# Kernel optimization log

Measured on AMD Instinct MI355X. Metric: run time of the kernel, lower is better.

## Reference

```python
import jax, jax.numpy as jnp
import numpy as np

N_NODES = 100000
N_EDGES = 3200000
IN_CH = 512
HIDDEN = 64
LOC_OUT = 16
OUT_CH = 40


def setup_inputs() -> dict:
    key = jax.random.key(0)
    ks = jax.random.split(key, 10)
    return {
        "batch_x": jax.random.normal(ks[0], (N_NODES, IN_CH), dtype=jnp.float32),
        "edge_index": jax.random.randint(ks[1], (2, N_EDGES), 0, N_NODES, dtype=jnp.int64),
        "glob_emb": jax.random.normal(ks[2], (N_NODES, LOC_OUT), dtype=jnp.float32),
        "W1": jax.random.normal(ks[3], (IN_CH, HIDDEN), dtype=jnp.float32) * (1.0 / np.sqrt(IN_CH)),
        "b1": jnp.zeros((HIDDEN,), dtype=jnp.float32),
        "W2": jax.random.normal(ks[4], (HIDDEN, LOC_OUT), dtype=jnp.float32) * (1.0 / np.sqrt(HIDDEN)),
        "b2": jnp.zeros((LOC_OUT,), dtype=jnp.float32),
        "att_w1": jax.random.normal(ks[5], (LOC_OUT, 16), dtype=jnp.float32) * 0.25,
        "att_b1": jnp.zeros((16,), dtype=jnp.float32),
        "att_w2": jax.random.normal(ks[6], (16, 1), dtype=jnp.float32) * 0.25,
        "lin1_w": jax.random.normal(ks[7], (LOC_OUT, OUT_CH), dtype=jnp.float32) * 0.25,
        "lin1_b": jnp.zeros((OUT_CH,), dtype=jnp.float32),
    }


def _gcn_conv(x, W, b, row, col, n):
    # GCNConv: out = D^-1/2 (A + I) D^-1/2 (X W) + b   (PyG default: self-loops, sym norm)
    h = x @ W
    loops = jnp.arange(n, dtype=row.dtype)
    row2 = jnp.concatenate([row, loops])  # sources (x_j)
    col2 = jnp.concatenate([col, loops])  # targets (aggregation index)
    deg = jax.ops.segment_sum(jnp.ones_like(col2, dtype=h.dtype), col2, num_segments=n)
    dinv = jax.lax.rsqrt(jnp.maximum(deg, 1.0))  # deg >= 1 thanks to self-loops
    norm = dinv[row2] * dinv[col2]               # [E+N]
    agg = jax.ops.segment_sum(h[row2] * norm[:, None], col2, num_segments=n)
    return agg + b


def reference(batch_x, edge_index, glob_emb, W1, b1, W2, b2, att_w1, att_b1, att_w2, lin1_w, lin1_b):
    n = batch_x.shape[0]
    row, col = edge_index[0], edge_index[1]
    x = _gcn_conv(batch_x, W1, b1, row, col, n)
    x = jax.nn.relu(x)  # dropout p=0.0 -> identity
    x = _gcn_conv(x, W2, b2, row, col, n)  # last layer: no relu/dropout
    z = jnp.stack([x, glob_emb], axis=1)  # [N, 2, 16]
    w = jnp.tanh(z @ att_w1 + att_b1) @ att_w2  # [N, 2, 1]
    beta = jax.nn.softmax(w, axis=1)
    emb = jnp.sum(beta * z, axis=1)  # [N, 16]
    return emb @ lin1_w + lin1_b  # [N, 40]
```

## Files before the change

### kernel.cpp

```cpp
#include <hip/hip_runtime.h>

#define N_IN 512
#define HID 64
#define NBLK 256

typedef __attribute__((ext_vector_type(4))) float f32x4;
typedef __attribute__((ext_vector_type(8))) short bf16x8;

__device__ inline float bf2f(unsigned short s) {
    union { unsigned int u; float f; } v; v.u = ((unsigned int)s) << 16; return v.f;
}
__device__ inline unsigned short f2bf(float f) {
    union { float f; unsigned int u; } v; v.f = f;
    unsigned int u = v.u;
    return (unsigned short)((u + 0x7FFFu + ((u >> 16) & 1u)) >> 16);
}

__global__ void k_detect(const int* __restrict__ EI, int* __restrict__ flag) {
    if (threadIdx.x == 0 && blockIdx.x == 0)
        *flag = (EI[1] == 0 && EI[3] == 0 && EI[5] == 0 && EI[7] == 0) ? 1 : 0;
}

__global__ __launch_bounds__(256) void k_histA(const int* __restrict__ EI, const int* __restrict__ flag,
                                               int* __restrict__ hist, int E, int N, int K) {
    extern __shared__ int hs[];
    for (int k = threadIdx.x; k < K; k += 256) hs[k] = 0;
    __syncthreads();
    int chunk = (E + NBLK - 1) / NBLK;
    int s = blockIdx.x * chunk, e = min(E, s + chunk);
    bool f = (*flag) != 0;
    for (int i = s + threadIdx.x; i < e; i += 256) {
        int c = f ? ((const int2*)EI)[E + i].x : EI[E + i];
        if ((unsigned)c < (unsigned)N) atomicAdd(&hs[c >> 8], 1);
    }
    __syncthreads();
    for (int k = threadIdx.x; k < K; k += 256) hist[k * NBLK + blockIdx.x] = hs[k];
}

__global__ __launch_bounds__(256) void k_scan_a2(const int* __restrict__ in, int* __restrict__ out,
                                                 int* __restrict__ bsum, int n) {
    __shared__ int sd[256];
    int i = blockIdx.x * 256 + threadIdx.x;
    int v = (i < n) ? in[i] : 0;
    sd[threadIdx.x] = v;
    __syncthreads();
    for (int off = 1; off < 256; off <<= 1) {
        int t = 0;
        if (threadIdx.x >= (unsigned)off) t = sd[threadIdx.x - off];
        __syncthreads();
        sd[threadIdx.x] += t;
        __syncthreads();
    }
    if (i < n) out[i] = sd[threadIdx.x] - v;
    if (threadIdx.x == 255) bsum[blockIdx.x] = sd[255];
}

__global__ __launch_bounds__(512) void k_scan_b(const int* __restrict__ bsum, int* __restrict__ bexc, int nb) {
    __shared__ int sd[512];
    int t = threadIdx.x;
    int v = (t < nb) ? bsum[t] : 0;
    sd[t] = v;
    __syncthreads();
    for (int off = 1; off < 512; off <<= 1) {
        int u = 0;
        if (t >= off) u = sd[t - off];
        __syncthreads();
        sd[t] += u;
        __syncthreads();
    }
    if (t < nb) bexc[t] = sd[t] - v;
    if (t == 511) bexc[nb] = sd[511];
}

__global__ __launch_bounds__(256) void k_scan_c2(const int* __restrict__ bexc, int* __restrict__ out,
                                                 int n, int nb) {
    int i = blockIdx.x * 256 + threadIdx.x;
    if (i < n) out[i] += bexc[blockIdx.x];
    if (i == 0) out[n] = bexc[nb];
}

__global__ __launch_bounds__(256) void k_partB(const int* __restrict__ EI, const int* __restrict__ flag,
                                               const int* __restrict__ histS, int* __restrict__ edges2,
                                               int E, int N, int K) {
    extern __shared__ int cur[];
    for (int k = threadIdx.x; k < K; k += 256) cur[k] = histS[k * NBLK + blockIdx.x];
    __syncthreads();
    int chunk = (E + NBLK - 1) / NBLK;
    int s = blockIdx.x * chunk, e = min(E, s + chunk);
    bool f = (*flag) != 0;
    for (int i = s + threadIdx.x; i < e; i += 256) {
        int r, c;
        if (f) { const int2* E2 = (const int2*)EI; r = E2[i].x; c = E2[E + i].x; }
        else   { r = EI[i]; c = EI[E + i]; }
        if ((unsigned)r >= (unsigned)N || (unsigned)c >= (unsigned)N) continue;
        int pos = atomicAdd(&cur[c >> 8], 1);
        edges2[pos] = r | ((c & 255) << 20);
    }
}

__global__ __launch_bounds__(256) void k_bucket(const int* __restrict__ histS, const int* __restrict__ edges2,
                                                int* __restrict__ edges, int* __restrict__ start,
                                                float* __restrict__ dinv, int N, int NBtot) {
    __shared__ int hist[256], sd[256], cur[256];
    int b = blockIdx.x, tid = threadIdx.x;
    int base = histS[b * NBLK];
    int end  = histS[(b + 1) * NBLK];
    hist[tid] = 0;
    __syncthreads();
    for (int i = base + tid; i < end; i += 256)
        atomicAdd(&hist[(edges2[i] >> 20) & 255], 1);
    __syncthreads();
    int v = hist[tid];
    sd[tid] = v;
    __syncthreads();
    for (int off = 1; off < 256; off <<= 1) {
        int t = 0;
        if (tid >= off) t = sd[tid - off];
        __syncthreads();
        sd[tid] += t;
        __syncthreads();
    }
    int excl = sd[tid] - v;
    cur[tid] = excl;
    int node = b * 256 + tid;
    if (node < N) {
        start[node] = base + excl;
        dinv[node] = rsqrtf((float)(v + 1));
    }
    if (b == 0 && tid == 0) start[N] = histS[NBtot];
    __syncthreads();
    for (int i = base + tid; i < end; i += 256) {
        int pv = edges2[i];
        int pos = atomicAdd(&cur[(pv >> 20) & 255], 1);
        edges[base + pos] = pv & 0xFFFFF;
    }
}

__global__ __launch_bounds__(256) void k_wt(const float* __restrict__ W, unsigned short* __restrict__ Wt) {
    int i = blockIdx.x * 256 + threadIdx.x;
    int k = i >> 6, n = i & 63;
    Wt[n * 512 + k] = f2bf(W[i]);
}

__global__ __launch_bounds__(256) void k_gemm1(const float* __restrict__ X, const unsigned short* __restrict__ Wt,
                                               const float* __restrict__ dinv, unsigned short* __restrict__ H, int N) {
    int tid = threadIdx.x;
    int w = tid >> 6, lane = tid & 63;
    int m_l = lane & 15, q = lane >> 4;
    int m0 = blockIdx.x * 128 + w * 32;
    int rA0 = m0 + m_l, rA1 = m0 + 16 + m_l;
    int rc0 = rA0 < N ? rA0 : N - 1;
    int rc1 = rA1 < N ? rA1 : N - 1;
    const float* baseA0 = X + (size_t)rc0 * 512 + q * 8;
    const float* baseA1 = X + (size_t)rc1 * 512 + q * 8;
    const unsigned short* baseB = Wt + (size_t)m_l * 512 + q * 8;

    f32x4 acc[2][4] = {};
#pragma unroll 4
    for (int c = 0; c < 16; ++c) {
        int ko = c * 32;
        float4 x0a = *(const float4*)(baseA0 + ko);
        float4 x0b = *(const float4*)(baseA0 + ko + 4);
        float4 x1a = *(const float4*)(baseA1 + ko);
        float4 x1b = *(const float4*)(baseA1 + ko + 4);
        bf16x8 a0, a1;
        a0[0] = (short)f2bf(x0a.x); a0[1] = (short)f2bf(x0a.y); a0[2] = (short)f2bf(x0a.z); a0[3] = (short)f2bf(x0a.w);
        a0[4] = (short)f2bf(x0b.x); a0[5] = (short)f2bf(x0b.y); a0[6] = (short)f2bf(x0b.z); a0[7] = (short)f2bf(x0b.w);
        a1[0] = (short)f2bf(x1a.x); a1[1] = (short)f2bf(x1a.y); a1[2] = (short)f2bf(x1a.z); a1[3] = (short)f2bf(x1a.w);
        a1[4] = (short)f2bf(x1b.x); a1[5] = (short)f2bf(x1b.y); a1[6] = (short)f2bf(x1b.z); a1[7] = (short)f2bf(x1b.w);
#pragma unroll
        for (int t = 0; t < 4; ++t) {
            bf16x8 b = *(const bf16x8*)(baseB + (size_t)t * 16 * 512 + ko);
            acc[0][t] = __builtin_amdgcn_mfma_f32_16x16x32_bf16(a0, b, acc[0][t], 0, 0, 0);
            acc[1][t] = __builtin_amdgcn_mfma_f32_16x16x32_bf16(a1, b, acc[1][t], 0, 0, 0);
        }
    }
#pragma unroll
    for (int h = 0; h < 2; ++h) {
#pragma unroll
        for (int rg = 0; rg < 4; ++rg) {
            int row = m0 + h * 16 + q * 4 + rg;
            if (row < N) {
                float dv = dinv[row];
#pragma unroll
                for (int t = 0; t < 4; ++t)
                    H[(size_t)row * 64 + t * 16 + m_l] = f2bf(acc[h][t][rg] * dv);
            }
        }
    }
}

__global__ __launch_bounds__(256) void k_agg1(const unsigned short* __restrict__ H, const int* __restrict__ edges,
                                              const int* __restrict__ start, const float* __restrict__ dinv,
                                              const float* __restrict__ b1, unsigned short* __restrict__ X1, int N) {
    int wid = blockIdx.x * 4 + (threadIdx.x >> 6);
    int lane = threadIdx.x & 63;
    if (wid >= N) return;
    int g = lane >> 4;
    int c4 = lane & 15;
    const size_t coff = (size_t)c4 * 4;
    float a0 = 0.f, a1 = 0.f, a2 = 0.f, a3 = 0.f;
    int s = start[wid], e = start[wid + 1];
    int i = s;
    if ((i & 3) && i < e) {
        int lim = min(e, (i + 3) & ~3);
        int j = i + g;
        if (j < lim) {
            uint2 v = *(const uint2*)(H + (size_t)edges[j] * 64 + coff);
            a0 += __uint_as_float(v.x << 16);
            a1 += __uint_as_float(v.x & 0xffff0000u);
            a2 += __uint_as_float(v.y << 16);
            a3 += __uint_as_float(v.y & 0xffff0000u);
        }
        i = lim;
    }
    for (; i + 16 <= e; i += 16) {
        int4 sv = *(const int4*)(edges + i + g * 4);
        uint2 v0 = *(const uint2*)(H + (size_t)sv.x * 64 + coff);
        uint2 v1 = *(const uint2*)(H + (size_t)sv.y * 64 + coff);
        uint2 v2 = *(const uint2*)(H + (size_t)sv.z * 64 + coff);
        uint2 v3 = *(const uint2*)(H + (size_t)sv.w * 64 + coff);
        a0 += __uint_as_float(v0.x << 16) + __uint_as_float(v1.x << 16)
            + __uint_as_float(v2.x << 16) + __uint_as_float(v3.x << 16);
        a1 += __uint_as_float(v0.x & 0xffff0000u) + __uint_as_float(v1.x & 0xffff0000u)
            + __uint_as_float(v2.x & 0xffff0000u) + __uint_as_float(v3.x & 0xffff0000u);
        a2 += __uint_as_float(v0.y << 16) + __uint_as_float(v1.y << 16)
            + __uint_as_float(v2.y << 16) + __uint_as_float(v3.y << 16);
        a3 += __uint_as_float(v0.y & 0xffff0000u) + __uint_as_float(v1.y & 0xffff0000u)
            + __uint_as_float(v2.y & 0xffff0000u) + __uint_as_float(v3.y & 0xffff0000u);
    }
    for (; i < e; i += 4) {
        int j = i + g;
        if (j < e) {
            uint2 v = *(const uint2*)(H + (size_t)edges[j] * 64 + coff);
            a0 += __uint_as_float(v.x << 16);
            a1 += __uint_as_float(v.x & 0xffff0000u);
            a2 += __uint_as_float(v.y << 16);
            a3 += __uint_as_float(v.y & 0xffff0000u);
        }
    }
    a0 += __shfl_xor(a0, 16, 64); a0 += __shfl_xor(a0, 32, 64);
    a1 += __shfl_xor(a1, 16, 64); a1 += __shfl_xor(a1, 32, 64);
    a2 += __shfl_xor(a2, 16, 64); a2 += __shfl_xor(a2, 32, 64);
    a3 += __shfl_xor(a3, 16, 64); a3 += __shfl_xor(a3, 32, 64);
    if (g == 0) {
        float dv = dinv[wid];
        uint2 sv = *(const uint2*)(H + (size_t)wid * 64 + coff);
        a0 += __uint_as_float(sv.x << 16);
        a1 += __uint_as_float(sv.x & 0xffff0000u);
        a2 += __uint_as_float(sv.y << 16);
        a3 += __uint_as_float(sv.y & 0xffff0000u);
        float4 bv = *(const float4*)(b1 + c4 * 4);
        ushort4 o;
        o.x = f2bf(fmaxf(a0 * dv + bv.x, 0.f));
        o.y = f2bf(fmaxf(a1 * dv + bv.y, 0.f));
        o.z = f2bf(fmaxf(a2 * dv + bv.z, 0.f));
        o.w = f2bf(fmaxf(a3 * dv + bv.w, 0.f));
        *(ushort4*)(X1 + (size_t)wid * 64 + coff) = o;
    }
}

__global__ __launch_bounds__(256) void k_gemm2(const unsigned short* __restrict__ X1, const float* __restrict__ W2,
                                               const float* __restrict__ dinv, unsigned short* __restrict__ H2, int N) {
    __shared__ float Ws[1024];
    __shared__ float Xs[64][68];
    int tid = threadIdx.x;
    for (int i = tid; i < 1024; i += 256) Ws[i] = W2[i];
    int m0 = blockIdx.x * 64;
#pragma unroll
    for (int j = 0; j < 4; ++j) {
        int f = (j * 256 + tid) * 4;
        int r = f >> 6, k = f & 63;
        uint2 v = make_uint2(0u, 0u);
        if (m0 + r < N) v = *(const uint2*)(X1 + (size_t)(m0 + r) * 64 + k);
        Xs[r][k + 0] = bf2f((unsigned short)(v.x & 0xffffu));
        Xs[r][k + 1] = bf2f((unsigned short)(v.x >> 16));
        Xs[r][k + 2] = bf2f((unsigned short)(v.y & 0xffffu));
        Xs[r][k + 3] = bf2f((unsigned short)(v.y >> 16));
    }
    __syncthreads();
    int r = tid >> 2, cq = tid & 3;
    float acc0 = 0.f, acc1 = 0.f, acc2 = 0.f, acc3 = 0.f;
#pragma unroll 8
    for (int k = 0; k < 64; ++k) {
        float xv = Xs[r][k];
        const float* wp = &Ws[k * 16 + cq * 4];
        acc0 += xv * wp[0]; acc1 += xv * wp[1]; acc2 += xv * wp[2]; acc3 += xv * wp[3];
    }
    int m = m0 + r;
    if (m < N) {
        float dv = dinv[m];
        ushort4 o; o.x = f2bf(acc0 * dv); o.y = f2bf(acc1 * dv); o.z = f2bf(acc2 * dv); o.w = f2bf(acc3 * dv);
        *(ushort4*)(H2 + (size_t)m * 16 + cq * 4) = o;
    }
}

__global__ __launch_bounds__(256) void k_agg2(const unsigned short* __restrict__ H2, const int* __restrict__ edges,
                                              const int* __restrict__ start, const float* __restrict__ dinv,
                                              const float* __restrict__ b2, float* __restrict__ X2, int N) {
    int wid = blockIdx.x * 4 + (threadIdx.x >> 6);
    int lane = threadIdx.x & 63;
    if (wid >= N) return;
    int g = lane >> 3;
    int c2 = lane & 7;
    const size_t coff = (size_t)c2 * 2;
    float a0 = 0.f, a1 = 0.f;
    int s = start[wid], e = start[wid + 1];
    int i = s;
    if ((i & 3) && i < e) {
        int lim = min(e, (i + 3) & ~3);
        int j = i + g;
        if (j < lim) {
            unsigned int v = *(const unsigned int*)(H2 + (size_t)edges[j] * 16 + coff);
            a0 += __uint_as_float(v << 16);
            a1 += __uint_as_float(v & 0xffff0000u);
        }
        i = lim;
    }
    for (; i + 32 <= e; i += 32) {
        int4 sv = *(const int4*)(edges + i + g * 4);
        unsigned int v0 = *(const unsigned int*)(H2 + (size_t)sv.x * 16 + coff);
        unsigned int v1 = *(const unsigned int*)(H2 + (size_t)sv.y * 16 + coff);
        unsigned int v2 = *(const unsigned int*)(H2 + (size_t)sv.z * 16 + coff);
        unsigned int v3 = *(const unsigned int*)(H2 + (size_t)sv.w * 16 + coff);
        a0 += __uint_as_float(v0 << 16) + __uint_as_float(v1 << 16)
            + __uint_as_float(v2 << 16) + __uint_as_float(v3 << 16);
        a1 += __uint_as_float(v0 & 0xffff0000u) + __uint_as_float(v1 & 0xffff0000u)
            + __uint_as_float(v2 & 0xffff0000u) + __uint_as_float(v3 & 0xffff0000u);
    }
    for (; i < e; i += 8) {
        int j = i + g;
        if (j < e) {
            unsigned int v = *(const unsigned int*)(H2 + (size_t)edges[j] * 16 + coff);
            a0 += __uint_as_float(v << 16);
            a1 += __uint_as_float(v & 0xffff0000u);
        }
    }
    a0 += __shfl_xor(a0, 8, 64); a0 += __shfl_xor(a0, 16, 64); a0 += __shfl_xor(a0, 32, 64);
    a1 += __shfl_xor(a1, 8, 64); a1 += __shfl_xor(a1, 16, 64); a1 += __shfl_xor(a1, 32, 64);
    if (g == 0) {
        float dv = dinv[wid];
        unsigned int sv = *(const unsigned int*)(H2 + (size_t)wid * 16 + coff);
        a0 += __uint_as_float(sv << 16);
        a1 += __uint_as_float(sv & 0xffff0000u);
        float2 bv = *(const float2*)(b2 + c2 * 2);
        float2 o; o.x = a0 * dv + bv.x; o.y = a1 * dv + bv.y;
        *(float2*)(X2 + (size_t)wid * 16 + coff) = o;
    }
}

__global__ __launch_bounds__(256) void k_head(const float* __restrict__ X2, const float* __restrict__ G,
                                              const float* __restrict__ AW1, const float* __restrict__ AB1,
                                              const float* __restrict__ AW2, const float* __restrict__ LW,
                                              const float* __restrict__ LB, float* __restrict__ OUT, int N) {
    __shared__ float s_aw1[256], s_ab1[16], s_aw2[16], s_lw[640], s_lb[40];
    int tid = threadIdx.x;
    s_aw1[tid] = AW1[tid];
    if (tid < 16) { s_ab1[tid] = AB1[tid]; s_aw2[tid] = AW2[tid]; }
    for (int i = tid; i < 640; i += 256) s_lw[i] = LW[i];
    if (tid < 40) s_lb[tid] = LB[tid];
    __syncthreads();
    int node = blockIdx.x * 256 + tid;
    if (node >= N) return;
    float x[16], g[16];
    const float4* xp = (const float4*)(X2 + (size_t)node * 16);
    const float4* gp = (const float4*)(G + (size_t)node * 16);
#pragma unroll
    for (int q = 0; q < 4; ++q) {
        float4 v = xp[q]; x[q*4] = v.x; x[q*4+1] = v.y; x[q*4+2] = v.z; x[q*4+3] = v.w;
        float4 u = gp[q]; g[q*4] = u.x; g[q*4+1] = u.y; g[q*4+2] = u.z; g[q*4+3] = u.w;
    }
    float wx = 0.f, wg = 0.f;
#pragma unroll
    for (int j = 0; j < 16; ++j) {
        float tx = s_ab1[j], tg = s_ab1[j];
#pragma unroll
        for (int c = 0; c < 16; ++c) { tx += x[c] * s_aw1[c*16 + j]; tg += g[c] * s_aw1[c*16 + j]; }
        wx += tanhf(tx) * s_aw2[j];
        wg += tanhf(tg) * s_aw2[j];
    }
    float m = fmaxf(wx, wg);
    float ex = expf(wx - m), eg = expf(wg - m);
    float inv = 1.f / (ex + eg);
    float bx = ex * inv, bg = eg * inv;
    float emb[16];
#pragma unroll
    for (int c = 0; c < 16; ++c) emb[c] = bx * x[c] + bg * g[c];
    float* op = OUT + (size_t)node * 40;
    for (int o = 0; o < 40; ++o) {
        float a = s_lb[o];
#pragma unroll
        for (int c = 0; c < 16; ++c) a += emb[c] * s_lw[c*40 + o];
        op[o] = a;
    }
}

extern "C" void kernel_launch(void* const* d_in, const int* in_sizes, int n_in,
                              void* d_out, int out_size, void* d_ws, size_t ws_size,
                              hipStream_t stream) {
    const float* X   = (const float*)d_in[0];
    const int*   EI  = (const int*)d_in[1];
    const float* G   = (const float*)d_in[2];
    const float* W1  = (const float*)d_in[3];
    const float* B1  = (const float*)d_in[4];
    const float* W2  = (const float*)d_in[5];
    const float* B2  = (const float*)d_in[6];
    const float* AW1 = (const float*)d_in[7];
    const float* AB1 = (const float*)d_in[8];
    const float* AW2 = (const float*)d_in[9];
    const float* LW  = (const float*)d_in[10];
    const float* LB  = (const float*)d_in[11];
    float* OUT = (float*)d_out;

    const int N = in_sizes[0] / N_IN;
    const int E = in_sizes[1] / 2;
    const int NB = (N + 255) / 256;
    const int K  = NB;
    const int NH = K * NBLK;
    const int SB = (NH + 255) / 256;

    char* w = (char*)d_ws;
    size_t off = 0;
    auto take = [&](size_t bytes) -> void* {
        void* p = (void*)(w + off);
        off = (off + bytes + 255) & ~(size_t)255;
        return p;
    };
    int*   flag   = (int*)take(16);
    int*   hist   = (int*)take((size_t)NH * 4);
    int*   histS  = (int*)take((size_t)(NH + 1) * 4);
    int*   bsum   = (int*)take((size_t)SB * 4);
    int*   bexc   = (int*)take((size_t)(SB + 1) * 4);
    int*   startp = (int*)take((size_t)(N + 1) * 4);
    float* dinvp  = (float*)take((size_t)N * 4);
    int*   edges2 = (int*)take((size_t)E * 4);
    int*   edges  = (int*)take((size_t)E * 4);
    unsigned short* wt = (unsigned short*)take((size_t)N_IN * HID * 2);
    unsigned short* h1 = (unsigned short*)take((size_t)N * 64 * 2);
    unsigned short* x1 = (unsigned short*)take((size_t)N * 64 * 2);
    unsigned short* h2 = (unsigned short*)take((size_t)N * 16 * 2);
    float* x2 = (float*)take((size_t)N * 16 * 4);
    (void)ws_size; (void)n_in; (void)out_size;

    k_detect <<<1, 64, 0, stream>>>(EI, flag);
    k_histA  <<<NBLK, 256, K * 4, stream>>>(EI, flag, hist, E, N, K);
    k_scan_a2<<<SB, 256, 0, stream>>>(hist, histS, bsum, NH);
    k_scan_b <<<1, 512, 0, stream>>>(bsum, bexc, SB);
    k_scan_c2<<<SB, 256, 0, stream>>>(bexc, histS, NH, SB);
    k_partB  <<<NBLK, 256, K * 4, stream>>>(EI, flag, histS, edges2, E, N, K);
    k_bucket <<<K, 256, 0, stream>>>(histS, edges2, edges, startp, dinvp, N, NH);
    k_wt     <<<(N_IN * HID + 255) / 256, 256, 0, stream>>>(W1, wt);
    k_gemm1  <<<(N + 127) / 128, 256, 0, stream>>>(X, wt, dinvp, h1, N);
    k_agg1   <<<(N + 3) / 4, 256, 0, stream>>>(h1, edges, startp, dinvp, B1, x1, N);
    k_gemm2  <<<(N + 63) / 64, 256, 0, stream>>>(x1, W2, dinvp, h2, N);
    k_agg2   <<<(N + 3) / 4, 256, 0, stream>>>(h2, edges, startp, dinvp, B2, x2, N);
    k_head   <<<NB, 256, 0, stream>>>(x2, G, AW1, AB1, AW2, LW, LB, OUT, N);
}
```

Before: 577.0 us.

## Merge graph-build and GEMM kernels, fuse agg1 with GEMM2, defer dinv scaling

Folds edge-layout detection into the histogram kernel and adds W1 transpose blocks to the same launch. Runs the edge partition concurrently with GEMM1 in one launch by making GEMM1 independent of dinv, then applies the dinv row scaling to H1 inside the bucket kernel. Fuses the first aggregation with the 64x16 second GEMM through warp shuffles, which removes the X1 intermediate and two launches. The trade-offs are an extra read-modify-write pass over H1, a second bf16 rounding of H1, and heterogeneous blocks inside one launch that could load-balance poorly.

New measurement: 582.2 us. Within noise of the previous version (+0.9%).

```diff
diff --git a/kernel.cpp b/kernel.cpp
--- a/kernel.cpp
+++ b/kernel.cpp
@@ -16,19 +16,23 @@
     return (unsigned short)((u + 0x7FFFu + ((u >> 16) & 1u)) >> 16);
 }
 
-__global__ void k_detect(const int* __restrict__ EI, int* __restrict__ flag) {
-    if (threadIdx.x == 0 && blockIdx.x == 0)
-        *flag = (EI[1] == 0 && EI[3] == 0 && EI[5] == 0 && EI[7] == 0) ? 1 : 0;
-}
-
-__global__ __launch_bounds__(256) void k_histA(const int* __restrict__ EI, const int* __restrict__ flag,
-                                               int* __restrict__ hist, int E, int N, int K) {
-    extern __shared__ int hs[];
+__global__ __launch_bounds__(256) void k_histA_wt(const int* __restrict__ EI, int* __restrict__ hist,
+                                                  const float* __restrict__ W1, unsigned short* __restrict__ Wt,
+                                                  int E, int N, int K) {
+    if (blockIdx.x >= NBLK) {
+        int i = (blockIdx.x - NBLK) * 256 + threadIdx.x;
+        int k = i >> 6, n = i & 63;
+        Wt[n * 512 + k] = f2bf(W1[i]);
+        return;
+    }
+    __shared__ int hs[512];
+    __shared__ int sflag;
+    if (threadIdx.x == 0) sflag = (EI[1] == 0 && EI[3] == 0 && EI[5] == 0 && EI[7] == 0) ? 1 : 0;
     for (int k = threadIdx.x; k < K; k += 256) hs[k] = 0;
     __syncthreads();
+    bool f = sflag != 0;
     int chunk = (E + NBLK - 1) / NBLK;
     int s = blockIdx.x * chunk, e = min(E, s + chunk);
-    bool f = (*flag) != 0;
     for (int i = s + threadIdx.x; i < e; i += 256) {
         int c = f ? ((const int2*)EI)[E + i].x : EI[E + i];
         if ((unsigned)c < (unsigned)N) atomicAdd(&hs[c >> 8], 1);
@@ -79,75 +83,35 @@
     if (i == 0) out[n] = bexc[nb];
 }
 
-__global__ __launch_bounds__(256) void k_partB(const int* __restrict__ EI, const int* __restrict__ flag,
-                                               const int* __restrict__ histS, int* __restrict__ edges2,
-                                               int E, int N, int K) {
-    extern __shared__ int cur[];
-    for (int k = threadIdx.x; k < K; k += 256) cur[k] = histS[k * NBLK + blockIdx.x];
-    __syncthreads();
-    int chunk = (E + NBLK - 1) / NBLK;
-    int s = blockIdx.x * chunk, e = min(E, s + chunk);
-    bool f = (*flag) != 0;
-    for (int i = s + threadIdx.x; i < e; i += 256) {
-        int r, c;
-        if (f) { const int2* E2 = (const int2*)EI; r = E2[i].x; c = E2[E + i].x; }
-        else   { r = EI[i]; c = EI[E + i]; }
-        if ((unsigned)r >= (unsigned)N || (unsigned)c >= (unsigned)N) continue;
-        int pos = atomicAdd(&cur[c >> 8], 1);
-        edges2[pos] = r | ((c & 255) << 20);
-    }
-}
-
-__global__ __launch_bounds__(256) void k_bucket(const int* __restrict__ histS, const int* __restrict__ edges2,
-                                                int* __restrict__ edges, int* __restrict__ start,
-                                                float* __restrict__ dinv, int N, int NBtot) {
-    __shared__ int hist[256], sd[256], cur[256];
-    int b = blockIdx.x, tid = threadIdx.x;
-    int base = histS[b * NBLK];
-    int end  = histS[(b + 1) * NBLK];
-    hist[tid] = 0;
-    __syncthreads();
-    for (int i = base + tid; i < end; i += 256)
-        atomicAdd(&hist[(edges2[i] >> 20) & 255], 1);
-    __syncthreads();
-    int v = hist[tid];
-    sd[tid] = v;
-    __syncthreads();
-    for (int off = 1; off < 256; off <<= 1) {
-        int t = 0;
-        if (tid >= off) t = sd[tid - off];
-        __syncthreads();
-        sd[tid] += t;
-        __syncthreads();
-    }
-    int excl = sd[tid] - v;
-    cur[tid] = excl;
-    int node = b * 256 + tid;
-    if (node < N) {
-        start[node] = base + excl;
-        dinv[node] = rsqrtf((float)(v + 1));
-    }
-    if (b == 0 && tid == 0) start[N] = histS[NBtot];
-    __syncthreads();
-    for (int i = base + tid; i < end; i += 256) {
-        int pv = edges2[i];
-        int pos = atomicAdd(&cur[(pv >> 20) & 255], 1);
-        edges[base + pos] = pv & 0xFFFFF;
-    }
-}
-
-__global__ __launch_bounds__(256) void k_wt(const float* __restrict__ W, unsigned short* __restrict__ Wt) {
-    int i = blockIdx.x * 256 + threadIdx.x;
-    int k = i >> 6, n = i & 63;
-    Wt[n * 512 + k] = f2bf(W[i]);
-}
-
-__global__ __launch_bounds__(256) void k_gemm1(const float* __restrict__ X, const unsigned short* __restrict__ Wt,
-                                               const float* __restrict__ dinv, unsigned short* __restrict__ H, int N) {
+__global__ __launch_bounds__(256) void k_partB_gemm1(const int* __restrict__ EI, const int* __restrict__ histS,
+                                                     int* __restrict__ edges2,
+                                                     const float* __restrict__ X, const unsigned short* __restrict__ Wt,
+                                                     unsigned short* __restrict__ H,
+                                                     int E, int N, int K) {
+    if (blockIdx.x < NBLK) {
+        __shared__ int cur[512];
+        __shared__ int sflag;
+        if (threadIdx.x == 0) sflag = (EI[1] == 0 && EI[3] == 0 && EI[5] == 0 && EI[7] == 0) ? 1 : 0;
+        for (int k = threadIdx.x; k < K; k += 256) cur[k] = histS[k * NBLK + blockIdx.x];
+        __syncthreads();
+        bool f = sflag != 0;
+        int chunk = (E + NBLK - 1) / NBLK;
+        int s = blockIdx.x * chunk, e = min(E, s + chunk);
+        for (int i = s + threadIdx.x; i < e; i += 256) {
+            int r, c;
+            if (f) { const int2* E2 = (const int2*)EI; r = E2[i].x; c = E2[E + i].x; }
+            else   { r = EI[i]; c = EI[E + i]; }
+            if ((unsigned)r >= (unsigned)N || (unsigned)c >= (unsigned)N) continue;
+            int pos = atomicAdd(&cur[c >> 8], 1);
+            edges2[pos] = r | ((c & 255) << 20);
+        }
+        return;
+    }
+    int bb = blockIdx.x - NBLK;
     int tid = threadIdx.x;
     int w = tid >> 6, lane = tid & 63;
     int m_l = lane & 15, q = lane >> 4;
-    int m0 = blockIdx.x * 128 + w * 32;
+    int m0 = bb * 128 + w * 32;
     int rA0 = m0 + m_l, rA1 = m0 + 16 + m_l;
     int rc0 = rA0 < N ? rA0 : N - 1;
     int rc1 = rA1 < N ? rA1 : N - 1;
@@ -181,20 +145,81 @@
         for (int rg = 0; rg < 4; ++rg) {
             int row = m0 + h * 16 + q * 4 + rg;
             if (row < N) {
-                float dv = dinv[row];
 #pragma unroll
                 for (int t = 0; t < 4; ++t)
-                    H[(size_t)row * 64 + t * 16 + m_l] = f2bf(acc[h][t][rg] * dv);
+                    H[(size_t)row * 64 + t * 16 + m_l] = f2bf(acc[h][t][rg]);
             }
         }
     }
 }
 
-__global__ __launch_bounds__(256) void k_agg1(const unsigned short* __restrict__ H, const int* __restrict__ edges,
-                                              const int* __restrict__ start, const float* __restrict__ dinv,
-                                              const float* __restrict__ b1, unsigned short* __restrict__ X1, int N) {
-    int wid = blockIdx.x * 4 + (threadIdx.x >> 6);
-    int lane = threadIdx.x & 63;
+__global__ __launch_bounds__(256) void k_bucket(const int* __restrict__ histS, const int* __restrict__ edges2,
+                                                int* __restrict__ edges, int* __restrict__ start,
+                                                float* __restrict__ dinv, unsigned short* __restrict__ H,
+                                                int N, int NBtot) {
+    __shared__ int hist[256], sd[256], cur[256];
+    __shared__ float dvs[256];
+    int b = blockIdx.x, tid = threadIdx.x;
+    int base = histS[b * NBLK];
+    int end  = histS[(b + 1) * NBLK];
+    hist[tid] = 0;
+    __syncthreads();
+    for (int i = base + tid; i < end; i += 256)
+        atomicAdd(&hist[(edges2[i] >> 20) & 255], 1);
+    __syncthreads();
+    int v = hist[tid];
+    sd[tid] = v;
+    __syncthreads();
+    for (int off = 1; off < 256; off <<= 1) {
+        int t = 0;
+        if (tid >= off) t = sd[tid - off];
+        __syncthreads();
+        sd[tid] += t;
+        __syncthreads();
+    }
+    int excl = sd[tid] - v;
+    cur[tid] = excl;
+    int node = b * 256 + tid;
+    float dvv = rsqrtf((float)(v + 1));
+    dvs[tid] = dvv;
+    if (node < N) {
+        start[node] = base + excl;
+        dinv[node] = dvv;
+    }
+    if (b == 0 && tid == 0) start[N] = histS[NBtot];
+    __syncthreads();
+    for (int i = base + tid; i < end; i += 256) {
+        int pv = edges2[i];
+        int pos = atomicAdd(&cur[(pv >> 20) & 255], 1);
+        edges[base + pos] = pv & 0xFFFFF;
+    }
+    for (int rr = tid >> 4; rr < 256; rr += 16) {
+        int n2 = b * 256 + rr;
+        if (n2 < N) {
+            float dv2 = dvs[rr];
+            uint2* pp = (uint2*)(H + (size_t)n2 * 64 + (size_t)(tid & 15) * 4);
+            uint2 vv = *pp;
+            float f0 = bf2f((unsigned short)(vv.x & 0xffffu)) * dv2;
+            float f1 = bf2f((unsigned short)(vv.x >> 16)) * dv2;
+            float f2 = bf2f((unsigned short)(vv.y & 0xffffu)) * dv2;
+            float f3 = bf2f((unsigned short)(vv.y >> 16)) * dv2;
+            vv.x = (unsigned int)f2bf(f0) | ((unsigned int)f2bf(f1) << 16);
+            vv.y = (unsigned int)f2bf(f2) | ((unsigned int)f2bf(f3) << 16);
+            *pp = vv;
+        }
+    }
+}
+
+__global__ __launch_bounds__(256) void k_agg1g2(const unsigned short* __restrict__ H, const int* __restrict__ edges,
+                                                const int* __restrict__ start, const float* __restrict__ dinv,
+                                                const float* __restrict__ b1, const float* __restrict__ W2,
+                                                unsigned short* __restrict__ H2, int N) {
+    __shared__ float w2s[64 * 17];
+    int tid = threadIdx.x;
+    for (int i = tid; i < 1024; i += 256) { int k = i >> 4, c = i & 15; w2s[k * 17 + c] = W2[i]; }
+    __syncthreads();
+    int wid = blockIdx.x * 4 + (tid >> 6);
+    int lane = tid & 63;
     if (wid >= N) return;
     int g = lane >> 4;
     int c4 = lane & 15;
@@ -243,56 +268,34 @@
     a1 += __shfl_xor(a1, 16, 64); a1 += __shfl_xor(a1, 32, 64);
     a2 += __shfl_xor(a2, 16, 64); a2 += __shfl_xor(a2, 32, 64);
     a3 += __shfl_xor(a3, 16, 64); a3 += __shfl_xor(a3, 32, 64);
-    if (g == 0) {
-        float dv = dinv[wid];
-        uint2 sv = *(const uint2*)(H + (size_t)wid * 64 + coff);
-        a0 += __uint_as_float(sv.x << 16);
-        a1 += __uint_as_float(sv.x & 0xffff0000u);
-        a2 += __uint_as_float(sv.y << 16);
-        a3 += __uint_as_float(sv.y & 0xffff0000u);
-        float4 bv = *(const float4*)(b1 + c4 * 4);
-        ushort4 o;
-        o.x = f2bf(fmaxf(a0 * dv + bv.x, 0.f));
-        o.y = f2bf(fmaxf(a1 * dv + bv.y, 0.f));
-        o.z = f2bf(fmaxf(a2 * dv + bv.z, 0.f));
-        o.w = f2bf(fmaxf(a3 * dv + bv.w, 0.f));
-        *(ushort4*)(X1 + (size_t)wid * 64 + coff) = o;
-    }
-}
-
-__global__ __launch_bounds__(256) void k_gemm2(const unsigned short* __restrict__ X1, const float* __restrict__ W2,
-                                               const float* __restrict__ dinv, unsigned short* __restrict__ H2, int N) {
-    __shared__ float Ws[1024];
-    __shared__ float Xs[64][68];
-    int tid = threadIdx.x;
-    for (int i = tid; i < 1024; i += 256) Ws[i] = W2[i];
-    int m0 = blockIdx.x * 64;
+    float dv = dinv[wid];
+    uint2 sv = *(const uint2*)(H + (size_t)wid * 64 + coff);
+    a0 += __uint_as_float(sv.x << 16);
+    a1 += __uint_as_float(sv.x & 0xffff0000u);
+    a2 += __uint_as_float(sv.y << 16);
+    a3 += __uint_as_float(sv.y & 0xffff0000u);
+    float4 bv = *(const float4*)(b1 + c4 * 4);
+    float r0 = fmaxf(a0 * dv + bv.x, 0.f);
+    float r1 = fmaxf(a1 * dv + bv.y, 0.f);
+    float r2 = fmaxf(a2 * dv + bv.z, 0.f);
+    float r3 = fmaxf(a3 * dv + bv.w, 0.f);
+    float p = 0.f;
 #pragma unroll
     for (int j = 0; j < 4; ++j) {
-        int f = (j * 256 + tid) * 4;
-        int r = f >> 6, k = f & 63;
-        uint2 v = make_uint2(0u, 0u);
-        if (m0 + r < N) v = *(const uint2*)(X1 + (size_t)(m0 + r) * 64 + k);
-        Xs[r][k + 0] = bf2f((unsigned short)(v.x & 0xffffu));
-        Xs[r][k + 1] = bf2f((unsigned short)(v.x >> 16));
-        Xs[r][k + 2] = bf2f((unsigned short)(v.y & 0xffffu));
-        Xs[r][k + 3] = bf2f((unsigned short)(v.y >> 16));
-    }
-    __syncthreads();
-    int r = tid >> 2, cq = tid & 3;
-    float acc0 = 0.f, acc1 = 0.f, acc2 = 0.f, acc3 = 0.f;
-#pragma unroll 8
-    for (int k = 0; k < 64; ++k) {
-        float xv = Xs[r][k];
-        const float* wp = &Ws[k * 16 + cq * 4];
-        acc0 += xv * wp[0]; acc1 += xv * wp[1]; acc2 += xv * wp[2]; acc3 += xv * wp[3];
-    }
-    int m = m0 + r;
-    if (m < N) {
-        float dv = dinv[m];
-        ushort4 o; o.x = f2bf(acc0 * dv); o.y = f2bf(acc1 * dv); o.z = f2bf(acc2 * dv); o.w = f2bf(acc3 * dv);
-        *(ushort4*)(H2 + (size_t)m * 16 + cq * 4) = o;
-    }
+        int src = 4 * g + j;
+        float x0 = __shfl(r0, src, 64);
+        float x1 = __shfl(r1, src, 64);
+        float x2 = __shfl(r2, src, 64);
+        float x3 = __shfl(r3, src, 64);
+        int kb = 16 * g + 4 * j;
+        p += x0 * w2s[(kb + 0) * 17 + c4];
+        p += x1 * w2s[(kb + 1) * 17 + c4];
+        p += x2 * w2s[(kb + 2) * 17 + c4];
+        p += x3 * w2s[(kb + 3) * 17 + c4];
+    }
+    p += __shfl_xor(p, 16, 64);
+    p += __shfl_xor(p, 32, 64);
+    if (g == 0) H2[(size_t)wid * 16 + c4] = f2bf(p * dv);
 }
 
 __global__ __launch_bounds__(256) void k_agg2(const unsigned short* __restrict__ H2, const int* __restrict__ edges,
@@ -418,6 +421,8 @@
     const int K  = NB;
     const int NH = K * NBLK;
     const int SB = (NH + 255) / 256;
+    const int WB = (N_IN * HID + 255) / 256;
+    const int GB = (N + 127) / 128;
 
     char* w = (char*)d_ws;
     size_t off = 0;
@@ -426,7 +431,6 @@
         off = (off + bytes + 255) & ~(size_t)255;
         return p;
     };
-    int*   flag   = (int*)take(16);
     int*   hist   = (int*)take((size_t)NH * 4);
     int*   histS  = (int*)take((size_t)(NH + 1) * 4);
     int*   bsum   = (int*)take((size_t)SB * 4);
@@ -437,22 +441,17 @@
     int*   edges  = (int*)take((size_t)E * 4);
     unsigned short* wt = (unsigned short*)take((size_t)N_IN * HID * 2);
     unsigned short* h1 = (unsigned short*)take((size_t)N * 64 * 2);
-    unsigned short* x1 = (unsigned short*)take((size_t)N * 64 * 2);
     unsigned short* h2 = (unsigned short*)take((size_t)N * 16 * 2);
     float* x2 = (float*)take((size_t)N * 16 * 4);
     (void)ws_size; (void)n_in; (void)out_size;
 
-    k_detect <<<1, 64, 0, stream>>>(EI, flag);
-    k_histA  <<<NBLK, 256, K * 4, stream>>>(EI, flag, hist, E, N, K);
-    k_scan_a2<<<SB, 256, 0, stream>>>(hist, histS, bsum, NH);
-    k_scan_b <<<1, 512, 0, stream>>>(bsum, bexc, SB);
-    k_scan_c2<<<SB, 256, 0, stream>>>(bexc, histS, NH, SB);
-    k_partB  <<<NBLK, 256, K * 4, stream>>>(EI, flag, histS, edges2, E, N, K);
-    k_bucket <<<K, 256, 0, stream>>>(histS, edges2, edges, startp, dinvp, N, NH);
-    k_wt     <<<(N_IN * HID + 255) / 256, 256, 0, stream>>>(W1, wt);
-    k_gemm1  <<<(N + 127) / 128, 256, 0, stream>>>(X, wt, dinvp, h1, N);
-    k_agg1   <<<(N + 3) / 4, 256, 0, stream>>>(h1, edges, startp, dinvp, B1, x1, N);
-    k_gemm2  <<<(N + 63) / 64, 256, 0, stream>>>(x1, W2, dinvp, h2, N);
-    k_agg2   <<<(N + 3) / 4, 256, 0, stream>>>(h2, edges, startp, dinvp, B2, x2, N);
-    k_head   <<<NB, 256, 0, stream>>>(x2, G, AW1, AB1, AW2, LW, LB, OUT, N);
-}
+    k_histA_wt   <<<NBLK + WB, 256, 0, stream>>>(EI, hist, W1, wt, E, N, K);
+    k_scan_a2    <<<SB, 256, 0, stream>>>(hist, histS, bsum, NH);
+    k_scan_b     <<<1, 512, 0, stream>>>(bsum, bexc, SB);
+    k_scan_c2    <<<SB, 256, 0, stream>>>(bexc, histS, NH, SB);
+    k_partB_gemm1<<<NBLK + GB, 256, 0, stream>>>(EI, histS, edges2, X, wt, h1, E, N, K);
+    k_bucket     <<<K, 256, 0, stream>>>(histS, edges2, edges, startp, dinvp, h1, N, NH);
+    k_agg1g2     <<<(N + 3) / 4, 256, 0, stream>>>(h1, edges, startp, dinvp, B1, W2, h2, N);
+    k_agg2       <<<(N + 3) / 4, 256, 0, stream>>>(h2, edges, startp, dinvp, B2, x2, N);
+    k_head       <<<NB, 256, 0, stream>>>(x2, G, AW1, AB1, AW2, LW, LB, OUT, N);
+}
```
